# Optimization experiments

Measured on AMD Instinct MI355X. Metric: run time of the kernel, lower is better.

## Reference

```python
import jax, jax.numpy as jnp
import numpy as np
import math

D_MODEL = 1024
N_HEADS = 16
D_KV = 64
NUM_BUCKETS = 32
MAX_DISTANCE = 128
BATCH = 4
SEQ = 2048


def _relative_position_bucket(relative_position, num_buckets=NUM_BUCKETS, max_distance=MAX_DISTANCE):
    # bidirectional=True (encoder)
    num_buckets //= 2
    relative_buckets = (relative_position > 0).astype(jnp.int32) * num_buckets
    rp = jnp.abs(relative_position)
    max_exact = num_buckets // 2
    is_small = rp < max_exact
    rp_safe = jnp.maximum(rp, 1)  # avoid log(0); masked by is_small anyway
    rp_if_large = max_exact + (
        jnp.log(rp_safe.astype(jnp.float32) / max_exact)
        / math.log(max_distance / max_exact)
        * (num_buckets - max_exact)
    ).astype(jnp.int32)
    rp_if_large = jnp.minimum(rp_if_large, num_buckets - 1)
    relative_buckets += jnp.where(is_small, rp, rp_if_large)
    return relative_buckets


def compute_bias(rel_bias, q_len, k_len):
    context = jnp.arange(q_len)[:, None]
    memory = jnp.arange(k_len)[None, :]
    buckets = _relative_position_bucket(memory - context)  # [q, k]
    values = rel_bias[buckets]                              # [q, k, h]
    return jnp.transpose(values, (2, 0, 1))[None]           # [1, h, q, k]


def setup_inputs() -> dict:
    key = jax.random.key(0)
    ks = jax.random.split(key, 6)
    s = 1.0 / math.sqrt(D_MODEL)
    return {
        "hidden_states": jax.random.normal(ks[0], (BATCH, SEQ, D_MODEL), jnp.float32),
        "wq": jax.random.normal(ks[1], (D_MODEL, N_HEADS * D_KV), jnp.float32) * s,
        "wk": jax.random.normal(ks[2], (D_MODEL, N_HEADS * D_KV), jnp.float32) * s,
        "wv": jax.random.normal(ks[3], (D_MODEL, N_HEADS * D_KV), jnp.float32) * s,
        "wo": jax.random.normal(ks[4], (N_HEADS * D_KV, D_MODEL), jnp.float32) * s,
        "rel_bias": jax.random.normal(ks[5], (NUM_BUCKETS, N_HEADS), jnp.float32) * 0.5,
    }


def reference(hidden_states, wq, wk, wv, wo, rel_bias):
    B, S, _ = hidden_states.shape

    def shape(x):  # [B,S,H*Dk] -> [B,H,S,Dk]
        return x.reshape(B, S, N_HEADS, D_KV).transpose(0, 2, 1, 3)

    q = shape(hidden_states @ wq)
    k = shape(hidden_states @ wk)
    v = shape(hidden_states @ wv)

    # NOTE: T5 does NOT scale by 1/sqrt(d_kv)
    scores = jnp.einsum("bhqd,bhkd->bhqk", q, k)
    position_bias = compute_bias(rel_bias, S, S)  # [1,H,S,S]
    scores = scores + position_bias
    attn = jax.nn.softmax(scores.astype(jnp.float32), axis=-1).astype(scores.dtype)
    ctx = jnp.einsum("bhqk,bhkd->bhqd", attn, v)
    ctx = ctx.transpose(0, 2, 1, 3).reshape(B, S, N_HEADS * D_KV)
    return ctx @ wo
```

## Files before the change

kernel.cpp:

```cpp
#include <hip/hip_runtime.h>
#include <hip/hip_bf16.h>

typedef unsigned short u16;
typedef unsigned int   u32;
typedef __bf16 bf16x8 __attribute__((ext_vector_type(8)));
typedef __bf16 bf16x4 __attribute__((ext_vector_type(4)));
typedef short  s16x4  __attribute__((ext_vector_type(4)));
typedef float  f32x4  __attribute__((ext_vector_type(4)));
typedef u16    u16x8  __attribute__((ext_vector_type(8)));
typedef u16    u16x4  __attribute__((ext_vector_type(4)));
typedef u32    u32x2  __attribute__((ext_vector_type(2)));

#define MFMA16(a,b,c) __builtin_amdgcn_mfma_f32_16x16x32_bf16(a,b,c,0,0,0)
#define LOG2E 1.4426950408889634f

__device__ __forceinline__ f32x4 mfma16k16(bf16x4 a, bf16x4 b, f32x4 c) {
#if __has_builtin(__builtin_amdgcn_mfma_f32_16x16x16bf16_1k)
    return __builtin_amdgcn_mfma_f32_16x16x16bf16_1k(
        __builtin_bit_cast(s16x4, a), __builtin_bit_cast(s16x4, b), c, 0, 0, 0);
#elif __has_builtin(__builtin_amdgcn_mfma_f32_16x16x16_bf16_1k)
    return __builtin_amdgcn_mfma_f32_16x16x16_bf16_1k(
        __builtin_bit_cast(s16x4, a), __builtin_bit_cast(s16x4, b), c, 0, 0, 0);
#else
    asm("v_mfma_f32_16x16x16_bf16 %0, %1, %2, %0" : "+v"(c) : "v"(a), "v"(b));
    return c;
#endif
}

__device__ __forceinline__ u16 f2b(float f) {
    u32 u = __builtin_bit_cast(u32, f);
    u32 r = (u + 0x7FFFu + ((u >> 16) & 1u)) >> 16;
    return (u16)r;
}

typedef const __attribute__((address_space(1))) u32* gaddr_t;
typedef __attribute__((address_space(3))) u32*       laddr_t;
__device__ __forceinline__ void gl_lds16(const void* g, void* l) {
    __builtin_amdgcn_global_load_lds((gaddr_t)g, (laddr_t)l, 16, 0, 0);
}

__global__ __launch_bounds__(256) void prep_kernel(
        const float* __restrict__ H, const float* __restrict__ wq,
        const float* __restrict__ wk, const float* __restrict__ wv,
        const float* __restrict__ wo, const float* __restrict__ rel_bias,
        u16* __restrict__ Hb, u16* __restrict__ Wt, u16* __restrict__ Wot,
        float* __restrict__ tab) {
    __shared__ u16 tile[64 * 72];
    int bi = blockIdx.x;
    int t = threadIdx.x;
    if (bi < 4096) {
        int i = (bi * 256 + t) * 8;
        float4 a = *(const float4*)(H + i);
        float4 b = *(const float4*)(H + i + 4);
        u16x8 o = { f2b(a.x), f2b(a.y), f2b(a.z), f2b(a.w),
                    f2b(b.x), f2b(b.y), f2b(b.z), f2b(b.w) };
        *(u16x8*)(Hb + i) = o;
    } else if (bi < 5120) {
        int g2 = bi - 4096;
        int g = g2 >> 8, rem = g2 & 255;
        int n0 = (rem >> 4) * 64, k0 = (rem & 15) * 64;
        const float* src = (g == 0) ? wq : (g == 1) ? wk : (g == 2) ? wv : wo;
        u16* dst = (g < 3) ? (Wt + g * 1048576) : Wot;
#pragma unroll
        for (int rr = 0; rr < 4; ++rr) {
            int idx = rr * 256 + t;
            int kr = idx >> 4, c = idx & 15;
            float4 v = *(const float4*)(src + (k0 + kr) * 1024 + n0 + c * 4);
            u16x4 o = { f2b(v.x), f2b(v.y), f2b(v.z), f2b(v.w) };
            *(u16x4*)&tile[kr * 72 + c * 4] = o;
        }
        __syncthreads();
#pragma unroll
        for (int rr = 0; rr < 2; ++rr) {
            int idx = rr * 256 + t;
            int n = idx >> 3, c = idx & 7;
            u16x8 o;
#pragma unroll
            for (int j = 0; j < 8; ++j) o[j] = tile[(c * 8 + j) * 72 + n];
            *(u16x8*)(dst + (n0 + n) * 1024 + k0 + c * 8) = o;
        }
    } else {
        int i = (bi - 5120) * 256 + t;
        int h = i >> 12;
        int idx = i & 4095;
        int delta = idx - 2048;
        int bucket = (delta > 0) ? 16 : 0;
        int rp = delta < 0 ? -delta : delta;
        if (rp < 8) {
            bucket += rp;
        } else {
            double v = log((double)rp / 8.0) / log(16.0) * 8.0;
            int tt = (int)v;
            int b2 = 8 + tt;
            bucket += (b2 < 15) ? b2 : 15;
        }
        tab[h * 4096 + idx] = rel_bias[bucket * 16 + h] * LOG2E;
    }
}

template <int MODE>
__global__ __launch_bounds__(256) void gemm_bt(
        const u16* __restrict__ A, const u16* __restrict__ Bt, int K, int N,
        u16* __restrict__ q_out, u16* __restrict__ k_out, u16* __restrict__ v_out,
        float* __restrict__ f_out) {
    __shared__ u16 As[128 * 32];
    __shared__ u16 Bs[128 * 32];
    __shared__ u16 vt_tile[MODE == 0 ? 128 * 136 : 1];
    int t = threadIdx.x;
    int lane = t & 63, w = t >> 6;
    int wm = w & 1, wn = w >> 1;
    int ln = lane & 15, quad = lane >> 4;
    int bid = (int)blockIdx.x;
    int xcd = bid & 7;
    int r = bid >> 3;
    int by = r >> 3;
    int bxl = r & 7;
    int m0 = (xcd * 8 + bxl) * 128;
    int n0 = by * 128;
    const u16* Ab = A + m0 * K;
    const u16* Bb = Bt + n0 * K;
    f32x4 acc[4][4] = {};
    int nk = K >> 5;
    for (int kt = 0; kt < nk; ++kt) {
        int k0 = kt * 32;
#pragma unroll
        for (int rr = 0; rr < 2; ++rr) {
            int idx = rr * 256 + t;
            int row = idx >> 2, c = (idx & 3) ^ (row & 3);
            gl_lds16(Ab + row * K + k0 + c * 8, ((char*)As) + idx * 16);
            gl_lds16(Bb + row * K + k0 + c * 8, ((char*)Bs) + idx * 16);
        }
        __syncthreads();
        bf16x8 af[4], bfr[4];
#pragma unroll
        for (int mb = 0; mb < 4; ++mb) {
            int row = wm * 64 + mb * 16 + ln;
            af[mb] = *(const bf16x8*)&As[row * 32 + ((quad ^ (row & 3)) << 3)];
        }
#pragma unroll
        for (int nb = 0; nb < 4; ++nb) {
            int row = wn * 64 + nb * 16 + ln;
            bfr[nb] = *(const bf16x8*)&Bs[row * 32 + ((quad ^ (row & 3)) << 3)];
        }
#pragma unroll
        for (int mb = 0; mb < 4; ++mb)
#pragma unroll
            for (int nb = 0; nb < 4; ++nb)
                acc[mb][nb] = MFMA16(af[mb], bfr[nb], acc[mb][nb]);
        __syncthreads();
    }
    if (MODE == 0 && n0 >= 2048) {
#pragma unroll
        for (int mb = 0; mb < 4; ++mb)
#pragma unroll
            for (int nb = 0; nb < 4; ++nb)
#pragma unroll
                for (int r2 = 0; r2 < 4; ++r2) {
                    int np = wn * 64 + nb * 16 + ln;
                    int mp = wm * 64 + mb * 16 + quad * 4 + r2;
                    vt_tile[np * 136 + mp] = f2b(acc[mb][nb][r2]);
                }
        __syncthreads();
        int h0 = (n0 >> 6) & 15;
        int b = m0 >> 11;
        int s0 = m0 & 2047;
#pragma unroll
        for (int j = 0; j < 8; ++j) {
            int e = j * 256 + t;
            int d_all = e >> 4;
            int sc = e & 15;
            int hh = h0 + (d_all >> 6);
            int d = d_all & 63;
            u16x8 val = *(const u16x8*)&vt_tile[d_all * 136 + sc * 8];
            *(u16x8*)(v_out + (b * 16 + hh) * 131072 + d * 2048 + s0 + sc * 8) = val;
        }
    } else {
#pragma unroll
        for (int mb = 0; mb < 4; ++mb)
#pragma unroll
            for (int nb = 0; nb < 4; ++nb)
#pragma unroll
                for (int r2 = 0; r2 < 4; ++r2) {
                    int m = m0 + wm * 64 + mb * 16 + quad * 4 + r2;
                    int n = n0 + wn * 64 + nb * 16 + ln;
                    float v = acc[mb][nb][r2];
                    if (MODE == 0) {
                        int which = n >> 10, h = (n >> 6) & 15, d = n & 63;
                        int b = m >> 11, s = m & 2047;
                        u16* dst = (which == 0) ? q_out : k_out;
                        float scale = (which == 0) ? LOG2E : 1.0f;
                        dst[(((b << 4) + h) * 2048 + s) * 64 + d] = f2b(v * scale);
                    } else {
                        f_out[m * N + n] = v;
                    }
                }
    }
}

__global__ __launch_bounds__(256, 4) void attn_kernel(
        const u16* __restrict__ Qb, const u16* __restrict__ Kb,
        const u16* __restrict__ Vt, const float* __restrict__ bias_tab,
        u16* __restrict__ ctx) {
    __shared__ u16 Ks[2][64 * 64];
    __shared__ u16 Vs[2][64 * 64];
    __shared__ float sb[384];
    int t = threadIdx.x;
    int lane = t & 63, w = t >> 6;
    int ln = lane & 15, quad = lane >> 4;
    int bid = blockIdx.x;
    int bh = (bid & 7) * 8 + (bid >> 7);
    int qtile = (bid >> 3) & 15;
    int h = bh & 15, b = bh >> 4;
    int q0 = qtile * 128;

    float chi = bias_tab[h * 4096 + 2048 + 1500];
    float clo = bias_tab[h * 4096 + 2048 - 1500];

    const float* tb = bias_tab + h * 4096 + 1857;
    for (int i = t; i < 384; i += 256) sb[i] = tb[i];

    const u16* qbase = Qb + (bh * 2048 + q0 + w * 16 + ln) * 64 + quad * 8;
    bf16x8 qf[2][2];
    qf[0][0] = *(const bf16x8*)(qbase);
    qf[0][1] = *(const bf16x8*)(qbase + 32);
    qf[1][0] = *(const bf16x8*)(qbase + 64 * 64);
    qf[1][1] = *(const bf16x8*)(qbase + 64 * 64 + 32);

    const u16* Kbase = Kb + bh * 2048 * 64;
    const u16* Vbase = Vt + bh * 64 * 2048;

    f32x4 oacc[2][4] = {};
    float l0 = 0.0f, l1 = 0.0f;
    int cb2_base = 191 - w * 16 + quad * 4 - ln;

    auto stage = [&](int kb, int bufidx) {
#pragma unroll
        for (int it = 0; it < 2; ++it) {
            int idx = it * 256 + t;
            int row = idx >> 3, c = (idx & 7) ^ (row & 7);
            gl_lds16(Kbase + (kb + row) * 64 + c * 8,
                     ((char*)&Ks[bufidx][0]) + idx * 16);
            gl_lds16(Vbase + row * 2048 + kb + c * 8,
                     ((char*)&Vs[bufidx][0]) + idx * 16);
        }
    };

    auto compute = [&](int kb0, const u16* Kc, const u16* Vc) {
        f32x4 sacc[2][4];
        int diffs[2] = {kb0 - q0, kb0 - q0 - 64};
        __builtin_amdgcn_s_setprio(1);
#pragma unroll
        for (int nb = 0; nb < 4; ++nb) {
            int key = nb * 16 + ln;
            int sw = key & 7;
            bf16x8 kf0 = *(const bf16x8*)&Kc[key * 64 + ((quad ^ sw) << 3)];
            bf16x8 kf1 = *(const bf16x8*)&Kc[key * 64 + (((quad ^ 4) ^ sw) << 3)];
#pragma unroll
            for (int g = 0; g < 2; ++g) {
                int diff = diffs[g];
                f32x4 ci;
                if (diff >= 192 || diff <= -192) {
                    float c0 = (diff > 0) ? chi : clo;
                    ci = {c0, c0, c0, c0};
                } else {
                    const float* bp = &sb[diff + cb2_base + nb * 16];
                    ci = {bp[0], bp[1], bp[2], bp[3]};
                }
                f32x4 scc = MFMA16(kf0, qf[g][0], ci);
                sacc[g][nb] = MFMA16(kf1, qf[g][1], scc);
            }
        }
        __builtin_amdgcn_s_setprio(0);

        bf16x4 pb[2][4];
#pragma unroll
        for (int g = 0; g < 2; ++g) {
            float s0 = 0.f, s1 = 0.f, s2 = 0.f, s3 = 0.f;
#pragma unroll
            for (int nb = 0; nb < 4; ++nb) {
                float e0 = __builtin_amdgcn_exp2f(sacc[g][nb][0]);
                float e1 = __builtin_amdgcn_exp2f(sacc[g][nb][1]);
                float e2 = __builtin_amdgcn_exp2f(sacc[g][nb][2]);
                float e3 = __builtin_amdgcn_exp2f(sacc[g][nb][3]);
                s0 += e0; s1 += e1; s2 += e2; s3 += e3;
                u32 lo, hi;
                asm("v_cvt_pk_bf16_f32 %0, %1, %2" : "=v"(lo) : "v"(e0), "v"(e1));
                asm("v_cvt_pk_bf16_f32 %0, %1, %2" : "=v"(hi) : "v"(e2), "v"(e3));
                u32x2 uv = {lo, hi};
                pb[g][nb] = __builtin_bit_cast(bf16x4, uv);
            }
            if (g == 0) l0 += (s0 + s1) + (s2 + s3);
            else        l1 += (s0 + s1) + (s2 + s3);
        }

        __builtin_amdgcn_s_setprio(1);
#pragma unroll
        for (int kc = 0; kc < 4; ++kc) {
            bf16x4 vA[4];
#pragma unroll
            for (int nd = 0; nd < 4; ++nd) {
                int d = nd * 16 + ln;
                int ch = (kc * 2 + (quad >> 1)) ^ (d & 7);
                vA[nd] = *(const bf16x4*)&Vc[d * 64 + (ch << 3) + ((quad & 1) << 2)];
            }
#pragma unroll
            for (int nd = 0; nd < 4; ++nd)
#pragma unroll
                for (int g = 0; g < 2; ++g)
                    oacc[g][nd] = mfma16k16(vA[nd], pb[g][kc], oacc[g][nd]);
        }
        __builtin_amdgcn_s_setprio(0);
    };

    stage(0, 0);
    asm volatile("s_waitcnt lgkmcnt(0)" ::: "memory");
    for (int kt = 0; kt < 31; ++kt) {
        int cur = kt & 1;
        stage((kt + 1) * 64, cur ^ 1);
        asm volatile("s_waitcnt vmcnt(4)" ::: "memory");
        __builtin_amdgcn_sched_barrier(0);
        __builtin_amdgcn_s_barrier();
        compute(kt * 64, &Ks[cur][0], &Vs[cur][0]);
        __builtin_amdgcn_s_barrier();
    }
    asm volatile("s_waitcnt vmcnt(0)" ::: "memory");
    __builtin_amdgcn_sched_barrier(0);
    __builtin_amdgcn_s_barrier();
    compute(31 * 64, &Ks[1][0], &Vs[1][0]);

    l0 += __shfl_xor(l0, 16); l0 += __shfl_xor(l0, 32);
    l1 += __shfl_xor(l1, 16); l1 += __shfl_xor(l1, 32);
    float linv[2] = {1.0f / l0, 1.0f / l1};
#pragma unroll
    for (int g = 0; g < 2; ++g) {
        int q = q0 + g * 64 + w * 16 + ln;
        u16* cp = ctx + (b * 2048 + q) * 1024 + h * 64 + quad * 4;
#pragma unroll
        for (int nd = 0; nd < 4; ++nd) {
            u16x4 o = { f2b(oacc[g][nd][0] * linv[g]), f2b(oacc[g][nd][1] * linv[g]),
                        f2b(oacc[g][nd][2] * linv[g]), f2b(oacc[g][nd][3] * linv[g]) };
            *(u16x4*)(cp + nd * 16) = o;
        }
    }
}

extern "C" void kernel_launch(void* const* d_in, const int* in_sizes, int n_in,
                              void* d_out, int out_size, void* d_ws, size_t ws_size,
                              hipStream_t stream) {
    const float* H   = (const float*)d_in[0];
    const float* wq  = (const float*)d_in[1];
    const float* wk  = (const float*)d_in[2];
    const float* wv  = (const float*)d_in[3];
    const float* wo  = (const float*)d_in[4];
    const float* rel = (const float*)d_in[5];
    float* out = (float*)d_out;

    char* ws = (char*)d_ws;
    u16* Hb    = (u16*)(ws);
    u16* Wt    = (u16*)(ws + 16777216);
    u16* Wot   = (u16*)(ws + 23068672);
    u16* Qb    = (u16*)(ws + 25165824);
    u16* Kb    = (u16*)(ws + 41943040);
    u16* Vt    = (u16*)(ws + 58720256);
    float* bias_tab = (float*)(ws + 75497472);
    u16* ctx = Hb;

    prep_kernel<<<5376, 256, 0, stream>>>(H, wq, wk, wv, wo, rel, Hb, Wt, Wot, bias_tab);
    gemm_bt<0><<<1536, 256, 0, stream>>>(Hb, Wt, 1024, 3072, Qb, Kb, Vt, nullptr);
    attn_kernel<<<1024, 256, 0, stream>>>(Qb, Kb, Vt, bias_tab, ctx);
    gemm_bt<1><<<512, 256, 0, stream>>>(ctx, Wot, 1024, 1024, nullptr, nullptr, nullptr, out);
}
```

Before: 293.5 us.

## Double-buffer GEMM LDS tiles with async prefetch and cheaper bucket log

Turns the projection GEMM main loop into a two-stage software pipeline. The next K-tile is loaded into a second LDS buffer, carved from a shared pool that overlaps the V-transpose tile, while the current tile is multiplied. Partial vmcnt waits and raw barriers replace the full __syncthreads each iteration, and MFMA issue priority is raised. The bias-table setup also swaps double-precision log for __log2f, which could shift bucket boundaries at exact power-of-two distances.

```diff
diff --git a/kernel.cpp b/kernel.cpp
--- a/kernel.cpp
+++ b/kernel.cpp
@@ -89,8 +89,8 @@
         if (rp < 8) {
             bucket += rp;
         } else {
-            double v = log((double)rp / 8.0) / log(16.0) * 8.0;
-            int tt = (int)v;
+            float lv = __log2f((float)rp) - 3.0f;
+            int tt = (int)(lv * 2.0f);
             int b2 = 8 + tt;
             bucket += (b2 < 15) ? b2 : 15;
         }
@@ -103,9 +103,8 @@
         const u16* __restrict__ A, const u16* __restrict__ Bt, int K, int N,
         u16* __restrict__ q_out, u16* __restrict__ k_out, u16* __restrict__ v_out,
         float* __restrict__ f_out) {
-    __shared__ u16 As[128 * 32];
-    __shared__ u16 Bs[128 * 32];
-    __shared__ u16 vt_tile[MODE == 0 ? 128 * 136 : 1];
+    __shared__ char pool_raw[MODE == 0 ? 128 * 136 * 2 : 32768];
+    u16* vt_tile = (u16*)pool_raw;
     int t = threadIdx.x;
     int lane = t & 63, w = t >> 6;
     int wm = w & 1, wn = w >> 1;
@@ -121,16 +120,22 @@
     const u16* Bb = Bt + n0 * K;
     f32x4 acc[4][4] = {};
     int nk = K >> 5;
-    for (int kt = 0; kt < nk; ++kt) {
+
+    auto stage = [&](int kt, int buf) {
         int k0 = kt * 32;
+        char* Ad = pool_raw + buf * 8192;
+        char* Bd = pool_raw + 16384 + buf * 8192;
 #pragma unroll
         for (int rr = 0; rr < 2; ++rr) {
             int idx = rr * 256 + t;
             int row = idx >> 2, c = (idx & 3) ^ (row & 3);
-            gl_lds16(Ab + row * K + k0 + c * 8, ((char*)As) + idx * 16);
-            gl_lds16(Bb + row * K + k0 + c * 8, ((char*)Bs) + idx * 16);
-        }
-        __syncthreads();
+            gl_lds16(Ab + row * K + k0 + c * 8, Ad + idx * 16);
+            gl_lds16(Bb + row * K + k0 + c * 8, Bd + idx * 16);
+        }
+    };
+    auto compute = [&](int buf) {
+        const u16* As = (const u16*)(pool_raw + buf * 8192);
+        const u16* Bs = (const u16*)(pool_raw + 16384 + buf * 8192);
         bf16x8 af[4], bfr[4];
 #pragma unroll
         for (int mb = 0; mb < 4; ++mb) {
@@ -142,14 +147,31 @@
             int row = wn * 64 + nb * 16 + ln;
             bfr[nb] = *(const bf16x8*)&Bs[row * 32 + ((quad ^ (row & 3)) << 3)];
         }
+        __builtin_amdgcn_s_setprio(1);
 #pragma unroll
         for (int mb = 0; mb < 4; ++mb)
 #pragma unroll
             for (int nb = 0; nb < 4; ++nb)
                 acc[mb][nb] = MFMA16(af[mb], bfr[nb], acc[mb][nb]);
+        __builtin_amdgcn_s_setprio(0);
+    };
+
+    stage(0, 0);
+    for (int kt = 0; kt < nk - 1; ++kt) {
+        stage(kt + 1, (kt + 1) & 1);
+        asm volatile("s_waitcnt vmcnt(4)" ::: "memory");
+        __builtin_amdgcn_sched_barrier(0);
+        __builtin_amdgcn_s_barrier();
+        compute(kt & 1);
+        __builtin_amdgcn_s_barrier();
+    }
+    asm volatile("s_waitcnt vmcnt(0)" ::: "memory");
+    __builtin_amdgcn_sched_barrier(0);
+    __builtin_amdgcn_s_barrier();
+    compute((nk - 1) & 1);
+
+    if (MODE == 0 && n0 >= 2048) {
         __syncthreads();
-    }
-    if (MODE == 0 && n0 >= 2048) {
 #pragma unroll
         for (int mb = 0; mb < 4; ++mb)
 #pragma unroll
```

After: 272.2 us. -7.3%, faster.
